# Performance work log

Measured on AMD Instinct MI355X. Metric: run time of the kernel, lower is better.

## Reference

```python
import jax, jax.numpy as jnp
import numpy as np

B, N, H, W, C_OUT = 4, 480000, 1024, 1024, 64
PR = (0.0, -39.68, -3.0, 69.12, 39.68, 1.0)  # point cloud range [x0,y0,z0,x1,y1,z1]
BN_EPS = 1e-5


def setup_inputs():
    key = jax.random.key(0)
    ks = iter(jax.random.split(key, 48))
    bidx = jax.random.randint(next(ks), (N,), 0, B).astype(jnp.float32)
    px = jax.random.uniform(next(ks), (N,), minval=PR[0], maxval=PR[3])
    py = jax.random.uniform(next(ks), (N,), minval=PR[1], maxval=PR[4])
    pz = jax.random.uniform(next(ks), (N,), minval=PR[2], maxval=PR[5])
    pi = jax.random.uniform(next(ks), (N,))
    points = jnp.stack([bidx, px, py, pz, pi], axis=1)  # [N,5]

    def w(shape):
        return jax.random.normal(next(ks), shape, jnp.float32) * 0.1

    def bnp(c):
        return (1.0 + 0.1 * jax.random.normal(next(ks), (c,), jnp.float32),
                0.1 * jax.random.normal(next(ks), (c,), jnp.float32),
                0.1 * jax.random.normal(next(ks), (c,), jnp.float32),
                jax.random.uniform(next(ks), (c,), minval=0.5, maxval=1.5))

    g0, be0, m0, v0 = bnp(8)
    g1, be1, m1, v1 = bnp(16)
    g2, be2, m2, v2 = bnp(32)
    g3, be3, m3, v3 = bnp(C_OUT)
    return {
        'points': points, 'batch_size': B,
        'w0': w((8, 2, 3, 3)), 'b0': w((8,)),
        'g0': g0, 'be0': be0, 'm0': m0, 'v0': v0,
        'w1': w((16, 1, 3, 3)), 'b1': w((16,)),  # groups=8 conv: 16 out, 8 in groups
        'g1': g1, 'be1': be1, 'm1': m1, 'v1': v1,
        'wdw': w((16, 1, 3, 3)), 'bdw': w((16,)),
        'wpw': w((32, 16, 1, 1)), 'bpw': w((32,)),
        'g2': g2, 'be2': be2, 'm2': m2, 'v2': v2,
        'w3': w((C_OUT, 32, 3, 3)), 'b3': w((C_OUT,)),
        'g3': g3, 'be3': be3, 'm3': m3, 'v3': v3,
    }


def conv2d(x, wt, b, groups=1, pad=1):
    out = jax.lax.conv_general_dilated(
        x, wt, (1, 1), [(pad, pad), (pad, pad)],
        feature_group_count=groups,
        dimension_numbers=('NCHW', 'OIHW', 'NCHW'))
    return out + b[None, :, None, None]


def bn(x, g, be, m, v):
    s = g * jax.lax.rsqrt(v + BN_EPS)
    return x * s[None, :, None, None] + (be - m * s)[None, :, None, None]


def maxpool2(x):
    return jax.lax.reduce_window(x, -jnp.inf, jax.lax.max,
                                 (1, 1, 2, 2), (1, 1, 2, 2), 'VALID')


def channel_shuffle(x, groups):
    b, c, h, w = x.shape
    return x.reshape(b, groups, c // groups, h, w).transpose(0, 2, 1, 3, 4).reshape(b, c, h, w)


def rasterize(points, batch_size):
    # points: [N,5] = (batch_idx, x, y, z, intensity)
    x_scale = W / (PR[3] - PR[0])
    y_scale = H / (PR[4] - PR[1])
    # PR[0]==0 -> no x shift (matches the source's branch)
    xp = (points[:, 1] * x_scale).astype(jnp.int32)  # trunc toward zero like torch .to(int)
    yp = ((points[:, 2] + (PR[4] - PR[1]) / 2) * y_scale).astype(jnp.int32)
    valid = (xp >= 0) & (xp < W) & (yp >= 0) & (yp < H)
    bi = jnp.where(valid, points[:, 0].astype(jnp.int32), batch_size)  # invalid -> OOB, dropped
    xi = jnp.where(valid, xp, W)
    yi = jnp.where(valid, yp, H)
    bev_z = jnp.full((batch_size, H, W), -10.0, jnp.float32)
    bev_z = bev_z.at[bi, yi, xi].max(points[:, 3], mode='drop')
    bev_i = jnp.zeros((batch_size, H, W), jnp.float32)
    bev_i = bev_i.at[bi, yi, xi].max(points[:, 4], mode='drop')
    return jnp.stack([bev_z, bev_i], axis=1)  # [B,2,H,W]


def reference(points, batch_size, w0, b0, g0, be0, m0, v0, w1, b1, g1, be1, m1, v1,
              wdw, bdw, wpw, bpw, g2, be2, m2, v2, w3, b3, g3, be3, m3, v3):
    x = rasterize(points, batch_size)
    x = jax.nn.relu(bn(conv2d(x, w0, b0), g0, be0, m0, v0))          # x_conv1
    x = maxpool2(x)
    x = jax.nn.relu(bn(conv2d(x, w1, b1, groups=8), g1, be1, m1, v1))  # x_conv2
    x = maxpool2(x)
    x = conv2d(x, wdw, bdw, groups=16)      # depthwise
    x = channel_shuffle(x, 16)              # identity when groups==channels, kept for faithfulness
    x = conv2d(x, wpw, bpw, pad=0)          # pointwise 16->32
    x = jax.nn.relu(bn(x, g2, be2, m2, v2))
    x = jax.nn.relu(bn(conv2d(x, w3, b3), g3, be3, m3, v3))          # x_conv3
    x = maxpool2(x)                         # x_conv4 == spatial_features
    return x
```

## Files before the change

### kernel.cpp

```cpp
#include <hip/hip_runtime.h>
#include <cstddef>

#define H_IN 1024
#define W_IN 1024
#define BN_EPS 1e-5f

typedef float f32x4 __attribute__((ext_vector_type(4)));
typedef _Float16 f16x8 __attribute__((ext_vector_type(8)));

__device__ __forceinline__ void atomicMaxF(float* addr, float val) {
    if (val >= 0.0f) {
        atomicMax((int*)addr, __float_as_int(val));
    } else {
        atomicMin((unsigned int*)addr, __float_as_uint(val));
    }
}

__global__ void k_init_bev(float* __restrict__ bev) {
    size_t i = (size_t)blockIdx.x * blockDim.x + threadIdx.x;
    int plane = (int)((i >> 20) & 1);
    bev[i] = plane == 0 ? -10.0f : 0.0f;
}

__global__ void k_rasterize(const float* __restrict__ pts, float* __restrict__ bev, int n) {
    int i = blockIdx.x * blockDim.x + threadIdx.x;
    if (i >= n) return;
    float fb  = pts[(size_t)i*5+0];
    float px  = pts[(size_t)i*5+1];
    float py  = pts[(size_t)i*5+2];
    float pz  = pts[(size_t)i*5+3];
    float pit = pts[(size_t)i*5+4];
    const float XS = (float)(1024.0/69.12);
    const float YS = (float)(1024.0/79.36);
    int xp = (int)(px * XS);
    int yp = (int)((py + 39.68f) * YS);
    if (xp < 0 || xp >= W_IN || yp < 0 || yp >= H_IN) return;
    int b = (int)fb;
    size_t off = (size_t)(b*2) * (H_IN*(size_t)W_IN) + (size_t)yp*W_IN + xp;
    atomicMaxF(bev + off, pz);
    atomicMaxF(bev + off + (size_t)H_IN*W_IN, pit);
}

__global__ __launch_bounds__(256, 4) void k_conv1(
                        const float* __restrict__ bev, const float* __restrict__ w0,
                        const float* __restrict__ b0, const float* __restrict__ g0,
                        const float* __restrict__ be0, const float* __restrict__ m0,
                        const float* __restrict__ v0, _Float16* __restrict__ out) {
    __shared__ float wS[144];
    __shared__ float sS[8], tS[8];
    int t = threadIdx.x;
    if (t < 144) wS[t] = w0[t];
    if (t < 8) {
        float s = g0[t] / sqrtf(v0[t] + BN_EPS);
        sS[t] = s;
        tS[t] = (b0[t] - m0[t]) * s + be0[t];
    }
    __syncthreads();
    int idx = blockIdx.x * 256 + t;
    int x = idx & 511, y = (idx >> 9) & 511, b = idx >> 18;
    const float* base = bev + (size_t)b * 2 * H_IN * W_IN;
    float in[2][4][4];
    #pragma unroll
    for (int c = 0; c < 2; c++)
        #pragma unroll
        for (int r = 0; r < 4; r++) {
            int iy = 2*y - 1 + r;
            #pragma unroll
            for (int cc = 0; cc < 4; cc++) {
                int ix = 2*x - 1 + cc;
                in[c][r][cc] = (iy >= 0 && iy < H_IN && ix >= 0 && ix < W_IN)
                    ? base[(size_t)c*H_IN*W_IN + (size_t)iy*W_IN + ix] : 0.0f;
            }
        }
    _Float16* ob = out + (size_t)b * 8 * 512 * 512 + (size_t)y*512 + x;
    #pragma unroll
    for (int oc = 0; oc < 8; oc++) {
        float mx = 0.0f;
        #pragma unroll
        for (int py = 0; py < 2; py++)
            #pragma unroll
            for (int px = 0; px < 2; px++) {
                float acc = 0.0f;
                #pragma unroll
                for (int c = 0; c < 2; c++)
                    #pragma unroll
                    for (int kh = 0; kh < 3; kh++)
                        #pragma unroll
                        for (int kw = 0; kw < 3; kw++)
                            acc += in[c][py+kh][px+kw] * wS[((oc*2+c)*3+kh)*3+kw];
                acc = fmaxf(acc * sS[oc] + tS[oc], 0.0f);
                mx = fmaxf(mx, acc);
            }
        ob[(size_t)oc*512*512] = (_Float16)mx;
    }
}

__global__ __launch_bounds__(256, 4) void k_conv2(
                        const _Float16* __restrict__ x1, const float* __restrict__ w1,
                        const float* __restrict__ b1, const float* __restrict__ g1,
                        const float* __restrict__ be1, const float* __restrict__ m1,
                        const float* __restrict__ v1, float* __restrict__ out) {
    __shared__ float wS[144];
    __shared__ float sS[16], tS[16];
    int t = threadIdx.x;
    if (t < 144) wS[t] = w1[t];
    if (t < 16) {
        float s = g1[t] / sqrtf(v1[t] + BN_EPS);
        sS[t] = s;
        tS[t] = (b1[t] - m1[t]) * s + be1[t];
    }
    __syncthreads();
    int idx = blockIdx.x * 256 + t;
    int x = idx & 255, y = (idx >> 8) & 255, b = idx >> 16;
    const _Float16* base = x1 + (size_t)b * 8 * 512 * 512;
    float* ob = out + (size_t)b * 16 * 256 * 256 + (size_t)y*256 + x;
    #pragma unroll
    for (int g = 0; g < 8; g++) {
        float p[4][4];
        #pragma unroll
        for (int r = 0; r < 4; r++) {
            int iy = 2*y - 1 + r;
            #pragma unroll
            for (int c = 0; c < 4; c++) {
                int ix = 2*x - 1 + c;
                p[r][c] = (iy >= 0 && iy < 512 && ix >= 0 && ix < 512)
                    ? (float)base[(size_t)g*512*512 + (size_t)iy*512 + ix] : 0.0f;
            }
        }
        #pragma unroll
        for (int sub = 0; sub < 2; sub++) {
            int oc = g*2 + sub;
            float mx = 0.0f;
            #pragma unroll
            for (int py = 0; py < 2; py++)
                #pragma unroll
                for (int px = 0; px < 2; px++) {
                    float acc = 0.0f;
                    #pragma unroll
                    for (int kh = 0; kh < 3; kh++)
                        #pragma unroll
                        for (int kw = 0; kw < 3; kw++)
                            acc += p[py+kh][px+kw] * wS[(oc*3+kh)*3+kw];
                    acc = fmaxf(acc * sS[oc] + tS[oc], 0.0f);
                    mx = fmaxf(mx, acc);
                }
            ob[(size_t)oc*65536] = mx;
        }
    }
}

__global__ __launch_bounds__(256, 4) void k_dwpw(
                       const float* __restrict__ x2, const float* __restrict__ wdw,
                       const float* __restrict__ bdw, const float* __restrict__ wpw,
                       const float* __restrict__ bpw, const float* __restrict__ g2,
                       const float* __restrict__ be2, const float* __restrict__ m2,
                       const float* __restrict__ v2, _Float16* __restrict__ out) {
    __shared__ float patch[16*10*36];
    __shared__ float wdwS[144];
    __shared__ float bdwS[16];
    __shared__ float wpwS[512];
    __shared__ float sS[32], tS[32];
    int t = threadIdx.x;
    if (t < 144) wdwS[t] = wdw[t];
    if (t < 16) bdwS[t] = bdw[t];
    for (int i = t; i < 512; i += 256) wpwS[i] = wpw[i];
    if (t < 32) {
        float s = g2[t] / sqrtf(v2[t] + BN_EPS);
        sS[t] = s;
        tS[t] = (bpw[t] - m2[t]) * s + be2[t];
    }

    int bi = blockIdx.x;
    int tx = bi & 7, ty = (bi >> 3) & 31, b = bi >> 8;
    int x0 = tx * 32, y0 = ty * 8;
    const float* base = x2 + (size_t)b * 16 * 256 * 256;

    for (int i = t; i < 16*10*34; i += 256) {
        int ic = i / 340;
        int rem = i - ic * 340;
        int r = rem / 34, c = rem - r * 34;
        int gy = y0 - 1 + r, gx = x0 - 1 + c;
        patch[(ic*10 + r)*36 + c] =
            (gy >= 0 && gy < 256 && gx >= 0 && gx < 256)
                ? base[(size_t)ic*65536 + (size_t)gy*256 + gx] : 0.0f;
    }
    __syncthreads();

    int px = t & 31, pyy = t >> 5;
    int x = x0 + px, y = y0 + pyy;

    float dv[16];
    #pragma unroll
    for (int ic = 0; ic < 16; ic++) {
        float d = bdwS[ic];
        #pragma unroll
        for (int r = 0; r < 3; r++)
            #pragma unroll
            for (int c = 0; c < 3; c++)
                d += patch[(ic*10 + pyy + r)*36 + px + c] * wdwS[ic*9 + r*3 + c];
        dv[ic] = d;
    }

    _Float16* ob = out + ((size_t)((b*256 + y)*256 + x)) * 32;
    #pragma unroll
    for (int q = 0; q < 4; q++) {
        f16x8 ov;
        #pragma unroll
        for (int j = 0; j < 8; j++) {
            int oc = q*8 + j;
            float a = 0.0f;
            #pragma unroll
            for (int ic = 0; ic < 16; ic++)
                a += dv[ic] * wpwS[oc*16+ic];
            ov[j] = (_Float16)fmaxf(a*sS[oc] + tS[oc], 0.0f);
        }
        *(f16x8*)(ob + q*8) = ov;
    }
}

__global__ void k_wprep(const float* __restrict__ w3, const float* __restrict__ b3,
                        const float* __restrict__ g3, const float* __restrict__ be3,
                        const float* __restrict__ m3, const float* __restrict__ v3,
                        _Float16* __restrict__ wh, float* __restrict__ tv) {
    __shared__ float sSh[64];
    int t = threadIdx.x;
    if (t < 64) {
        float s = g3[t] / sqrtf(v3[t] + BN_EPS);
        sSh[t] = s;
        if (blockIdx.x == 0) tv[t] = (b3[t] - m3[t]) * s + be3[t];
    }
    __syncthreads();
    int khw = blockIdx.x;
    for (int i = t; i < 2048; i += 256) {
        int oc = i >> 5;
        wh[khw*2048 + i] = (_Float16)(w3[(size_t)i*9 + khw] * sSh[oc]);
    }
}

__global__ __launch_bounds__(256, 2) void k_conv3m(const _Float16* __restrict__ xh,
                                                   const _Float16* __restrict__ wh,
                                                   const float* __restrict__ tv,
                                                   float* __restrict__ out) {
    __shared__ _Float16 As[10*66*40];
    int t = threadIdx.x;
    int lane = t & 63, w = t >> 6;
    int l15 = lane & 15, l4 = lane >> 4;
    int bi = blockIdx.x;
    int xt = bi & 3, yg = (bi >> 2) & 31, b = bi >> 7;
    int x0 = xt * 64;
    int y0 = yg * 8;

    f16x8 Bf[9][4];
    #pragma unroll
    for (int khw = 0; khw < 9; khw++)
        #pragma unroll
        for (int g = 0; g < 4; g++)
            Bf[khw][g] = *(const f16x8*)(wh + ((khw*64 + g*16 + l15)*32 + 8*l4));

    float tvv[4];
    #pragma unroll
    for (int g = 0; g < 4; g++) tvv[g] = tv[g*16 + l15];

    for (int s = t; s < 660; s += 256) {
        int row = s / 66, px = s - row*66;
        int gy = y0 - 1 + row, gx = x0 - 1 + px;
        float4* dst = (float4*)&As[(row*66 + px)*40];
        if (gy >= 0 && gy < 256 && gx >= 0 && gx < 256) {
            const float4* src = (const float4*)(xh + ((size_t)((b*256 + gy)*256 + gx)) * 32);
            #pragma unroll
            for (int j = 0; j < 4; j++) dst[j] = src[j];
        } else {
            float4 z = make_float4(0.f, 0.f, 0.f, 0.f);
            #pragma unroll
            for (int j = 0; j < 4; j++) dst[j] = z;
        }
    }
    __syncthreads();

    for (int ti = 0; ti < 4; ti++) {
        int ypool = yg*4 + ti;
        f32x4 acc[2][4];
        #pragma unroll
        for (int f = 0; f < 2; f++)
            #pragma unroll
            for (int g = 0; g < 4; g++)
                acc[f][g] = (f32x4){0.f, 0.f, 0.f, 0.f};

        #pragma unroll
        for (int kh = 0; kh < 3; kh++)
            #pragma unroll
            for (int kw = 0; kw < 3; kw++) {
                f16x8 Af[2];
                #pragma unroll
                for (int f = 0; f < 2; f++) {
                    int row = 2*ti + f + kh;
                    int px = w*16 + l15 + kw;
                    Af[f] = *(const f16x8*)&As[(row*66 + px)*40 + 8*l4];
                }
                #pragma unroll
                for (int f = 0; f < 2; f++)
                    #pragma unroll
                    for (int g = 0; g < 4; g++)
                        acc[f][g] = __builtin_amdgcn_mfma_f32_16x16x32_f16(
                            Af[f], Bf[kh*3+kw][g], acc[f][g], 0, 0, 0);
            }

        #pragma unroll
        for (int g = 0; g < 4; g++) {
            int oc = g*16 + l15;
            #pragma unroll
            for (int q = 0; q < 2; q++) {
                float v0 = fmaxf(fmaxf(acc[0][g][2*q]   + tvv[g], 0.f),
                                 fmaxf(acc[0][g][2*q+1] + tvv[g], 0.f));
                float v1 = fmaxf(fmaxf(acc[1][g][2*q]   + tvv[g], 0.f),
                                 fmaxf(acc[1][g][2*q+1] + tvv[g], 0.f));
                int px = x0/2 + w*8 + 2*l4 + q;
                out[(((size_t)b*64 + oc)*128 + ypool)*128 + px] = fmaxf(v0, v1);
            }
        }
    }
}

extern "C" void kernel_launch(void* const* d_in, const int* in_sizes, int n_in,
                              void* d_out, int out_size, void* d_ws, size_t ws_size,
                              hipStream_t stream) {
    const float* points = (const float*)d_in[0];
    int n = in_sizes[0] / 5;
    const float* w0  = (const float*)d_in[2];
    const float* b0  = (const float*)d_in[3];
    const float* g0  = (const float*)d_in[4];
    const float* be0 = (const float*)d_in[5];
    const float* m0  = (const float*)d_in[6];
    const float* v0  = (const float*)d_in[7];
    const float* w1  = (const float*)d_in[8];
    const float* b1  = (const float*)d_in[9];
    const float* g1  = (const float*)d_in[10];
    const float* be1 = (const float*)d_in[11];
    const float* m1  = (const float*)d_in[12];
    const float* v1  = (const float*)d_in[13];
    const float* wdw = (const float*)d_in[14];
    const float* bdw = (const float*)d_in[15];
    const float* wpw = (const float*)d_in[16];
    const float* bpw = (const float*)d_in[17];
    const float* g2  = (const float*)d_in[18];
    const float* be2 = (const float*)d_in[19];
    const float* m2  = (const float*)d_in[20];
    const float* v2  = (const float*)d_in[21];
    const float* w3  = (const float*)d_in[22];
    const float* b3  = (const float*)d_in[23];
    const float* g3  = (const float*)d_in[24];
    const float* be3 = (const float*)d_in[25];
    const float* m3  = (const float*)d_in[26];
    const float* v3  = (const float*)d_in[27];

    float* ws  = (float*)d_ws;
    float* bev = ws;
    _Float16* x1h = (_Float16*)(ws + 8388608);
    float* x2  = ws;
    _Float16* x3h = (_Float16*)(ws + 8388608);
    _Float16* wh  = (_Float16*)(ws + 16777216);
    float* tv  = ws + 16786432;
    float* outp = (float*)d_out;

    k_wprep<<<9, 256, 0, stream>>>(w3, b3, g3, be3, m3, v3, wh, tv);
    k_init_bev<<<32768, 256, 0, stream>>>(bev);
    k_rasterize<<<(n + 255)/256, 256, 0, stream>>>(points, bev, n);
    k_conv1<<<4096, 256, 0, stream>>>(bev, w0, b0, g0, be0, m0, v0, x1h);
    k_conv2<<<1024, 256, 0, stream>>>(x1h, w1, b1, g1, be1, m1, v1, x2);
    k_dwpw<<<1024, 256, 0, stream>>>(x2, wdw, bdw, wpw, bpw, g2, be2, m2, v2, x3h);
    k_conv3m<<<512, 256, 0, stream>>>(x3h, wh, tv, outp);
}
```

Before: 147.0 us.

## Use order-preserving uint encoding and interleaved BEV layout with memset init

The BEV buffer becomes interleaved (z, intensity pairs per pixel) and stores an order-preserving unsigned encoding of each float. Rasterization then needs a single unsigned atomicMax per channel, with no sign branch. Zero means an untouched cell and is decoded to the -10 or 0 default. This lets the init kernel become a plain hipMemsetAsync and lets conv1 read both channels from adjacent addresses. It adds decode work in conv1 and depends on the empty-cell sentinel being handled correctly.

```diff
diff --git a/kernel.cpp b/kernel.cpp
--- a/kernel.cpp
+++ b/kernel.cpp
@@ -8,21 +8,17 @@
 typedef float f32x4 __attribute__((ext_vector_type(4)));
 typedef _Float16 f16x8 __attribute__((ext_vector_type(8)));
 
-__device__ __forceinline__ void atomicMaxF(float* addr, float val) {
-    if (val >= 0.0f) {
-        atomicMax((int*)addr, __float_as_int(val));
-    } else {
-        atomicMin((unsigned int*)addr, __float_as_uint(val));
-    }
-}
-
-__global__ void k_init_bev(float* __restrict__ bev) {
-    size_t i = (size_t)blockIdx.x * blockDim.x + threadIdx.x;
-    int plane = (int)((i >> 20) & 1);
-    bev[i] = plane == 0 ? -10.0f : 0.0f;
-}
-
-__global__ void k_rasterize(const float* __restrict__ pts, float* __restrict__ bev, int n) {
+__device__ __forceinline__ unsigned encF(float f) {
+    unsigned u = __float_as_uint(f);
+    return (u & 0x80000000u) ? ~u : (u | 0x80000000u);
+}
+__device__ __forceinline__ float decF(unsigned e, float untouched) {
+    if (e == 0u) return untouched;
+    unsigned bits = (e & 0x80000000u) ? (e ^ 0x80000000u) : ~e;
+    return __uint_as_float(bits);
+}
+
+__global__ void k_rasterize(const float* __restrict__ pts, unsigned* __restrict__ bev, int n) {
     int i = blockIdx.x * blockDim.x + threadIdx.x;
     if (i >= n) return;
     float fb  = pts[(size_t)i*5+0];
@@ -36,13 +32,13 @@
     int yp = (int)((py + 39.68f) * YS);
     if (xp < 0 || xp >= W_IN || yp < 0 || yp >= H_IN) return;
     int b = (int)fb;
-    size_t off = (size_t)(b*2) * (H_IN*(size_t)W_IN) + (size_t)yp*W_IN + xp;
-    atomicMaxF(bev + off, pz);
-    atomicMaxF(bev + off + (size_t)H_IN*W_IN, pit);
+    size_t off = (((size_t)b * H_IN + yp) * W_IN + xp) * 2;
+    atomicMax(bev + off,     encF(pz));
+    atomicMax(bev + off + 1, encF(pit));
 }
 
 __global__ __launch_bounds__(256, 4) void k_conv1(
-                        const float* __restrict__ bev, const float* __restrict__ w0,
+                        const unsigned* __restrict__ bev, const float* __restrict__ w0,
                         const float* __restrict__ b0, const float* __restrict__ g0,
                         const float* __restrict__ be0, const float* __restrict__ m0,
                         const float* __restrict__ v0, _Float16* __restrict__ out) {
@@ -58,20 +54,24 @@
     __syncthreads();
     int idx = blockIdx.x * 256 + t;
     int x = idx & 511, y = (idx >> 9) & 511, b = idx >> 18;
-    const float* base = bev + (size_t)b * 2 * H_IN * W_IN;
+    const unsigned* base = bev + (size_t)b * H_IN * W_IN * 2;
     float in[2][4][4];
     #pragma unroll
-    for (int c = 0; c < 2; c++)
-        #pragma unroll
-        for (int r = 0; r < 4; r++) {
-            int iy = 2*y - 1 + r;
-            #pragma unroll
-            for (int cc = 0; cc < 4; cc++) {
-                int ix = 2*x - 1 + cc;
-                in[c][r][cc] = (iy >= 0 && iy < H_IN && ix >= 0 && ix < W_IN)
-                    ? base[(size_t)c*H_IN*W_IN + (size_t)iy*W_IN + ix] : 0.0f;
-            }
-        }
+    for (int r = 0; r < 4; r++) {
+        int iy = 2*y - 1 + r;
+        #pragma unroll
+        for (int cc = 0; cc < 4; cc++) {
+            int ix = 2*x - 1 + cc;
+            if (iy >= 0 && iy < H_IN && ix >= 0 && ix < W_IN) {
+                const unsigned* p2 = base + ((size_t)iy*W_IN + ix)*2;
+                in[0][r][cc] = decF(p2[0], -10.0f);
+                in[1][r][cc] = decF(p2[1], 0.0f);
+            } else {
+                in[0][r][cc] = 0.0f;
+                in[1][r][cc] = 0.0f;
+            }
+        }
+    }
     _Float16* ob = out + (size_t)b * 8 * 512 * 512 + (size_t)y*512 + x;
     #pragma unroll
     for (int oc = 0; oc < 8; oc++) {
@@ -354,7 +354,7 @@
     const float* v3  = (const float*)d_in[27];
 
     float* ws  = (float*)d_ws;
-    float* bev = ws;
+    unsigned* bev = (unsigned*)ws;
     _Float16* x1h = (_Float16*)(ws + 8388608);
     float* x2  = ws;
     _Float16* x3h = (_Float16*)(ws + 8388608);
@@ -363,7 +363,7 @@
     float* outp = (float*)d_out;
 
     k_wprep<<<9, 256, 0, stream>>>(w3, b3, g3, be3, m3, v3, wh, tv);
-    k_init_bev<<<32768, 256, 0, stream>>>(bev);
+    hipMemsetAsync(bev, 0, (size_t)4 * H_IN * W_IN * 2 * sizeof(unsigned), stream);
     k_rasterize<<<(n + 255)/256, 256, 0, stream>>>(points, bev, n);
     k_conv1<<<4096, 256, 0, stream>>>(bev, w0, b0, g0, be0, m0, v0, x1h);
     k_conv2<<<1024, 256, 0, stream>>>(x1h, w1, b1, g1, be1, m1, v1, x2);
```

After: 151.7 us. 1.03x slower.
